# Kernel optimization log

Measured on AMD Instinct MI355X. Metric: run time of the kernel, lower is better.

Reference implementation:

```python
import jax, jax.numpy as jnp
import numpy as np

B, T, S, D, V, NX = 4, 256, 400, 512, 50000, 50
VEXT = V + NX  # extended vocab


def setup_inputs() -> dict:
    key = jax.random.key(0)
    ks = jax.random.split(key, 10)
    s = 0.02
    return {
        "x": jax.random.normal(ks[0], (B, T, D), dtype=jnp.float32),
        "enc_outputs": jax.random.normal(ks[1], (B, S, D), dtype=jnp.float32),
        "src_mask": jax.random.randint(ks[2], (B, 1, S), 0, 2, dtype=jnp.int32),
        "enc_batch_extend_vocab": jax.random.randint(ks[3], (B, S), 0, VEXT, dtype=jnp.int64),
        "extra_zeros": jnp.zeros((B, T, NX), dtype=jnp.float32),
        "fc_w": jax.random.normal(ks[4], (V, D), dtype=jnp.float32) * s,
        "fc_b": jnp.zeros((V,), dtype=jnp.float32),
        "pgen_w": jax.random.normal(ks[5], (1, D), dtype=jnp.float32) * s,
        "pgen_b": jnp.zeros((1,), dtype=jnp.float32),
        "wq": jax.random.normal(ks[6], (D, D), dtype=jnp.float32) * s,
        "bq": jnp.zeros((D,), dtype=jnp.float32),
        "wk": jax.random.normal(ks[7], (D, D), dtype=jnp.float32) * s,
        "bk": jnp.zeros((D,), dtype=jnp.float32),
    }


def reference(x, enc_outputs, src_mask, enc_batch_extend_vocab, extra_zeros,
              fc_w, fc_b, pgen_w, pgen_b, wq, bq, wk, bk):
    # vocab distribution: [B,T,V]
    p_vocab = jax.nn.softmax(x @ fc_w.T + fc_b, axis=-1)
    # single-head cross attention probs (h=1 -> d_k = D)
    q = x @ wq.T + bq                 # [B,T,D]
    k = enc_outputs @ wk.T + bk       # [B,S,D]
    scores = jnp.einsum('btd,bsd->bts', q, k) / jnp.sqrt(jnp.float32(D))
    scores = jnp.where(src_mask == 0, jnp.float32(-1e9), scores)  # mask [B,1,S]
    attn_probs = jax.nn.softmax(scores, axis=-1)  # [B,T,S]
    # generation gate
    p_gen = jax.nn.sigmoid(x @ pgen_w.T + pgen_b)  # [B,T,1]
    attn_dist = (1.0 - p_gen) * attn_probs         # copy distribution over source
    p_ext = jnp.concatenate([p_gen * p_vocab, extra_zeros], axis=-1)  # [B,T,VEXT]
    # scatter-add copy probs into extended vocab slots
    b_idx = jnp.arange(B)[:, None, None]
    t_idx = jnp.arange(T)[None, :, None]
    v_idx = enc_batch_extend_vocab[:, None, :]
    bb, tt, vv = jnp.broadcast_arrays(b_idx, t_idx, v_idx)  # each [B,T,S]
    p_ext = p_ext.at[bb, tt, vv].add(attn_dist)
    return jnp.log(jnp.maximum(p_ext, jnp.float32(1e-9)))
```

## Files before the change

### kernel.cpp

```cpp
#include <hip/hip_runtime.h>
#include <hip/hip_bf16.h>
#include <math.h>

constexpr int cB = 4, cT = 256, cS = 400, cD = 512, cV = 50000, cNX = 50;
constexpr int cVEXT = cV + cNX;
constexpr int cPAN  = (cV + 127) / 128;
constexpr int cMQ   = cB * cT;

typedef __attribute__((ext_vector_type(8))) short short8v;
typedef __attribute__((ext_vector_type(4))) float floatx4;

__device__ inline ushort f2bf(float f) {
    union { float f; unsigned u; } v; v.f = f;
    unsigned r = (v.u + 0x7FFFu + ((v.u >> 16) & 1u)) >> 16;
    return (ushort)r;
}

__global__ __launch_bounds__(256) void cast_kernel(
    const float* __restrict__ src, ushort* __restrict__ dst, int n4)
{
    const int stride = gridDim.x * 256;
    for (int i = blockIdx.x * 256 + threadIdx.x; i < n4; i += stride) {
        float4 v = *(const float4*)(src + (size_t)i * 4);
        ushort4 o;
        o.x = f2bf(v.x); o.y = f2bf(v.y); o.z = f2bf(v.z); o.w = f2bf(v.w);
        *(ushort4*)(dst + (size_t)i * 4) = o;
    }
}

template<bool STATS>
__global__ __launch_bounds__(256) void gemm2(
    const ushort* __restrict__ A, const ushort* __restrict__ Wb,
    const float* __restrict__ bias, float* __restrict__ Cf,
    float* __restrict__ pm, float* __restrict__ ps,
    int M, int N, int K, int ldc)
{
    __shared__ ushort As[2][128 * 32];
    __shared__ ushort Bs[2][128 * 32];
    __shared__ float sm_m[2][128];
    __shared__ float sm_s[2][128];

    const int tid  = threadIdx.x;
    const int lane = tid & 63;
    const int wv   = tid >> 6;
    const int wm   = wv >> 1;
    const int wn   = wv & 1;

    int bm, bn, pan = 0;
    if constexpr (STATS) {
        const int wg  = blockIdx.y * gridDim.x + blockIdx.x;
        const int nwg = gridDim.x * gridDim.y;
        const int j   = (wg & 7) * (nwg >> 3) + (wg >> 3);
        pan = j >> 3;
        bm  = (j & 7) * 128;
        bn  = pan * 128;
    } else {
        bm = blockIdx.x * 128;
        bn = blockIdx.y * 128;
    }

    const int srow = lane >> 2;
    const int sk   = (lane & 3) * 8;

    const int nt = K >> 5;

    floatx4 acc[4][4] = {};

    auto stage = [&](int bidx, int t) {
        const int k0 = t * 32;
        #pragma unroll
        for (int c = 0; c < 2; ++c) {
            const int lr = wv * 32 + c * 16;
            int ga = bm + lr + srow; if (ga >= M) ga = M - 1;
            __builtin_amdgcn_global_load_lds(
                (const __attribute__((address_space(1))) void*)(A + (size_t)ga * K + k0 + sk),
                (__attribute__((address_space(3))) void*)&As[bidx][lr * 32], 16, 0, 0);
        }
        #pragma unroll
        for (int c = 0; c < 2; ++c) {
            const int lr = wv * 32 + c * 16;
            int gb = bn + lr + srow; if (gb >= N) gb = N - 1;
            __builtin_amdgcn_global_load_lds(
                (const __attribute__((address_space(1))) void*)(Wb + (size_t)gb * K + k0 + sk),
                (__attribute__((address_space(3))) void*)&Bs[bidx][lr * 32], 16, 0, 0);
        }
    };

    stage(0, 0);
    __syncthreads();

    const int fr = lane & 15;
    const int g  = lane >> 4;
    int buf = 0;

    for (int t = 0; t < nt; ++t) {
        if (t + 1 < nt) stage(buf ^ 1, t + 1);
        short8v a[4], b[4];
        #pragma unroll
        for (int mi = 0; mi < 4; ++mi)
            a[mi] = *(const short8v*)&As[buf][(wm * 64 + mi * 16 + fr) * 32 + g * 8];
        #pragma unroll
        for (int ni = 0; ni < 4; ++ni)
            b[ni] = *(const short8v*)&Bs[buf][(wn * 64 + ni * 16 + fr) * 32 + g * 8];
        #pragma unroll
        for (int mi = 0; mi < 4; ++mi)
            #pragma unroll
            for (int ni = 0; ni < 4; ++ni)
                acc[mi][ni] = __builtin_amdgcn_mfma_f32_16x16x32_bf16(
                    a[mi], b[ni], acc[mi][ni], 0, 0, 0);
        __syncthreads();
        buf ^= 1;
    }

    float bv[4]; bool val[4];
    #pragma unroll
    for (int ni = 0; ni < 4; ++ni) {
        const int colg = bn + wn * 64 + ni * 16 + fr;
        val[ni] = (colg < N);
        bv[ni] = val[ni] ? bias[colg] : 0.f;
    }
    #pragma unroll
    for (int mi = 0; mi < 4; ++mi)
        #pragma unroll
        for (int ni = 0; ni < 4; ++ni)
            #pragma unroll
            for (int r = 0; r < 4; ++r)
                acc[mi][ni][r] += bv[ni];

    if constexpr (STATS) {
        #pragma unroll
        for (int mi = 0; mi < 4; ++mi) {
            #pragma unroll
            for (int r = 0; r < 4; ++r) {
                float mx = -1e30f;
                #pragma unroll
                for (int ni = 0; ni < 4; ++ni)
                    if (val[ni]) mx = fmaxf(mx, acc[mi][ni][r]);
                #pragma unroll
                for (int sw = 1; sw < 16; sw <<= 1)
                    mx = fmaxf(mx, __shfl_xor(mx, sw));
                float sm = 0.f;
                #pragma unroll
                for (int ni = 0; ni < 4; ++ni)
                    if (val[ni]) sm += __expf(acc[mi][ni][r] - mx);
                #pragma unroll
                for (int sw = 1; sw < 16; sw <<= 1)
                    sm += __shfl_xor(sm, sw);
                if (fr == 0) {
                    const int rl = wm * 64 + mi * 16 + g * 4 + r;
                    sm_m[wn][rl] = mx;
                    sm_s[wn][rl] = sm;
                }
            }
        }
        __syncthreads();
        if (tid < 128) {
            const float m0 = sm_m[0][tid], m1 = sm_m[1][tid];
            const float s0 = sm_s[0][tid], s1 = sm_s[1][tid];
            const float mm = fmaxf(m0, m1);
            const float ss = s0 * __expf(m0 - mm) + s1 * __expf(m1 - mm);
            const int grow = bm + tid;
            if (grow < M) {
                pm[(size_t)pan * M + grow] = mm;
                ps[(size_t)pan * M + grow] = ss;
            }
        }
    }

    #pragma unroll
    for (int mi = 0; mi < 4; ++mi) {
        #pragma unroll
        for (int ni = 0; ni < 4; ++ni) {
            if (!val[ni]) continue;
            const int colg = bn + wn * 64 + ni * 16 + fr;
            #pragma unroll
            for (int r = 0; r < 4; ++r) {
                const int row = bm + wm * 64 + mi * 16 + g * 4 + r;
                if (row < M) Cf[(size_t)row * ldc + colg] = acc[mi][ni][r];
            }
        }
    }
}

__global__ __launch_bounds__(256) void combine_kernel(
    const float* __restrict__ pm, const float* __restrict__ ps,
    const float* __restrict__ pgen, float* __restrict__ rowadd)
{
    const int lane = threadIdx.x & 63;
    const int wv   = threadIdx.x >> 6;
    const int row  = blockIdx.x * 64 + lane;

    float m = -1e30f, s = 0.f;
    #pragma unroll 2
    for (int i = wv; i < cPAN; i += 4) {
        const float mi = pm[(size_t)i * cMQ + row];
        const float si = ps[(size_t)i * cMQ + row];
        const float nm = fmaxf(m, mi);
        s = s * __expf(m - nm) + si * __expf(mi - nm);
        m = nm;
    }
    __shared__ float rm[4][64], rs[4][64];
    rm[wv][lane] = m; rs[wv][lane] = s;
    __syncthreads();
    if (wv == 0) {
        m = rm[0][lane]; s = rs[0][lane];
        #pragma unroll
        for (int i = 1; i < 4; ++i) {
            const float m2 = rm[i][lane], s2 = rs[i][lane];
            const float nm = fmaxf(m, m2);
            s = s * __expf(m - nm) + s2 * __expf(m2 - nm);
            m = nm;
        }
        rowadd[row] = __logf(pgen[row]) - m - __logf(s);
    }
}

__global__ __launch_bounds__(512) void transform_row(
    float* __restrict__ out, const float* __restrict__ rowadd,
    const int* __restrict__ ebev, const float* __restrict__ attn)
{
    const int row = blockIdx.x;
    const int b   = row / cT;
    const int tid = threadIdx.x;
    constexpr float LOGMIN = -20.72326583694641f;

    __shared__ int   pos[cS];
    __shared__ float add[cS];
    for (int s = tid; s < cS; s += 512) {
        pos[s] = ebev[b * cS + s];
        add[s] = attn[(size_t)row * cS + s];
    }

    const float a = rowadd[row];
    float2* rp = (float2*)(out + (size_t)row * cVEXT);
    constexpr int NF2 = cVEXT / 2;
    constexpr int NV2 = cV / 2;
    for (int i = tid; i < NF2; i += 512) {
        float2 o;
        if (i < NV2) {
            float2 v = rp[i];
            o.x = fmaxf(v.x + a, LOGMIN);
            o.y = fmaxf(v.y + a, LOGMIN);
        } else {
            o.x = LOGMIN; o.y = LOGMIN;
        }
        rp[i] = o;
    }
    __syncthreads();

    float* rowf = out + (size_t)row * cVEXT;
    for (int s = tid; s < cS; s += 512) {
        const int p = pos[s];
        bool leader = true;
        for (int s2 = 0; s2 < s; ++s2)
            if (pos[s2] == p) { leader = false; break; }
        if (!leader) continue;
        float sum = add[s];
        for (int s2 = s + 1; s2 < cS; ++s2)
            if (pos[s2] == p) sum += add[s2];
        const float base = __expf(rowf[p]);
        rowf[p] = __logf(fmaxf(base + sum, 1e-9f));
    }
}

__global__ __launch_bounds__(64) void pgen_kernel(
    const float* __restrict__ x, const float* __restrict__ w,
    const float* __restrict__ b, float* __restrict__ pgen)
{
    const int row = blockIdx.x;
    const int lane = threadIdx.x;
    const float* xr = x + (size_t)row * cD;
    float s = 0.f;
    for (int i = lane; i < cD; i += 64) s += xr[i] * w[i];
    #pragma unroll
    for (int off = 32; off; off >>= 1) s += __shfl_down(s, off);
    if (lane == 0) pgen[row] = 1.f / (1.f + __expf(-(s + b[0])));
}

__global__ __launch_bounds__(256) void attn_kernel(
    const float* __restrict__ q, const float* __restrict__ k,
    const int* __restrict__ src_mask, const float* __restrict__ pgen,
    float* __restrict__ attn)
{
    constexpr float scale = 0.04419417382415922f;
    const int row = blockIdx.x;
    const int b = row / cT;
    const int tid = threadIdx.x;

    __shared__ __align__(16) float qs[cD];
    __shared__ float sc[cS];
    __shared__ float red[4];

    for (int i = tid; i < cD; i += 256) qs[i] = q[(size_t)row * cD + i];
    __syncthreads();

    for (int s = tid; s < cS; s += 256) {
        const float* kr = k + ((size_t)b * cS + s) * cD;
        float dot = 0.f;
        #pragma unroll 4
        for (int i = 0; i < cD; i += 4) {
            float4 kv = *(const float4*)(kr + i);
            float4 qv = *(const float4*)(qs + i);
            dot += qv.x * kv.x + qv.y * kv.y + qv.z * kv.z + qv.w * kv.w;
        }
        float v = dot * scale;
        if (src_mask[b * cS + s] == 0) v = -1e9f;
        sc[s] = v;
    }
    __syncthreads();

    float m = -3.4e38f;
    for (int s = tid; s < cS; s += 256) m = fmaxf(m, sc[s]);
    #pragma unroll
    for (int off = 32; off; off >>= 1) m = fmaxf(m, __shfl_down(m, off));
    if ((tid & 63) == 0) red[tid >> 6] = m;
    __syncthreads();
    m = fmaxf(fmaxf(red[0], red[1]), fmaxf(red[2], red[3]));
    __syncthreads();

    float sum = 0.f;
    for (int s = tid; s < cS; s += 256) {
        float e = __expf(sc[s] - m);
        sc[s] = e;
        sum += e;
    }
    #pragma unroll
    for (int off = 32; off; off >>= 1) sum += __shfl_down(sum, off);
    if ((tid & 63) == 0) red[tid >> 6] = sum;
    __syncthreads();
    sum = red[0] + red[1] + red[2] + red[3];

    const float w = (1.f - pgen[row]) / sum;
    for (int s = tid; s < cS; s += 256)
        attn[(size_t)row * cS + s] = sc[s] * w;
}

extern "C" void kernel_launch(void* const* d_in, const int* in_sizes, int n_in,
                              void* d_out, int out_size, void* d_ws, size_t ws_size,
                              hipStream_t stream)
{
    const float* x      = (const float*)d_in[0];
    const float* enc    = (const float*)d_in[1];
    const int*   mask   = (const int*)d_in[2];
    const int*   ebev   = (const int*)d_in[3];
    const float* fc_w   = (const float*)d_in[5];
    const float* fc_b   = (const float*)d_in[6];
    const float* pgen_w = (const float*)d_in[7];
    const float* pgen_b = (const float*)d_in[8];
    const float* wq     = (const float*)d_in[9];
    const float* bq     = (const float*)d_in[10];
    const float* wk     = (const float*)d_in[11];
    const float* bk     = (const float*)d_in[12];
    float* out = (float*)d_out;

    float* ws     = (float*)d_ws;
    float* q      = ws;
    float* kbuf   = q + (size_t)cB * cT * cD;
    float* pgen   = kbuf + (size_t)cB * cS * cD;
    float* attn   = pgen + cB * cT;
    float* pm     = attn + (size_t)cB * cT * cS;
    float* ps     = pm + (size_t)cPAN * cMQ;
    float* rowadd = ps + (size_t)cPAN * cMQ;
    ushort* xb    = (ushort*)(rowadd + cMQ);
    ushort* encb  = xb + (size_t)cB * cT * cD;
    ushort* wqb   = encb + (size_t)cB * cS * cD;
    ushort* wkb   = wqb + (size_t)cD * cD;
    ushort* wb    = wkb + (size_t)cD * cD;

    const dim3 blk(256);
    const int MQ = cMQ;
    const int MK = cB * cS;

    cast_kernel<<<dim3(512), blk, 0, stream>>>(x, xb, (cB * cT * cD) / 4);
    cast_kernel<<<dim3(512), blk, 0, stream>>>(enc, encb, (cB * cS * cD) / 4);
    cast_kernel<<<dim3(256), blk, 0, stream>>>(wq, wqb, (cD * cD) / 4);
    cast_kernel<<<dim3(256), blk, 0, stream>>>(wk, wkb, (cD * cD) / 4);
    cast_kernel<<<dim3(2048), blk, 0, stream>>>(fc_w, wb, (cV * cD) / 4);

    gemm2<false><<<dim3(MQ / 128, cD / 128), blk, 0, stream>>>(
        xb, wqb, bq, q, nullptr, nullptr, MQ, cD, cD, cD);
    gemm2<false><<<dim3((MK + 127) / 128, cD / 128), blk, 0, stream>>>(
        encb, wkb, bk, kbuf, nullptr, nullptr, MK, cD, cD, cD);
    pgen_kernel<<<dim3(MQ), dim3(64), 0, stream>>>(x, pgen_w, pgen_b, pgen);

    attn_kernel<<<dim3(MQ), blk, 0, stream>>>(q, kbuf, mask, pgen, attn);

    gemm2<true><<<dim3(8, cPAN), blk, 0, stream>>>(
        xb, wb, fc_b, out, pm, ps, MQ, cV, cD, cVEXT);

    combine_kernel<<<dim3(MQ / 64), blk, 0, stream>>>(pm, ps, pgen, rowadd);

    transform_row<<<dim3(MQ), dim3(512), 0, stream>>>(out, rowadd, ebev, attn);
}
```

Baseline: 449.9 us.

## Store vocab logits as bf16 in upper half of output row and expand in place

The big vocab GEMM now writes its logits as bf16 into the upper half of each output row's byte range, halving that intermediate write. The transform kernel reads the bf16 values, applies the row offset and clamp, and writes fp32 results into the lower half of the same row. A block-wide barrier between each read and its write guards against overlapping positions in the same row. The GEMM shared-memory staging is also changed to a chunked layout, so each lane loads its MFMA fragment contiguously. Risks are bf16 rounding of the logits before the log output, and correctness that depends on the in-place aliasing order.

Result: no change. 443.5 us (-1.4%).

```diff
diff --git a/kernel.cpp b/kernel.cpp
--- a/kernel.cpp
+++ b/kernel.cpp
@@ -5,6 +5,8 @@
 constexpr int cB = 4, cT = 256, cS = 400, cD = 512, cV = 50000, cNX = 50;
 constexpr int cVEXT = cV + cNX;
 constexpr int cPAN  = (cV + 127) / 128;
+constexpr int cCBLD = cVEXT * 2;
+constexpr int cTOP  = 50100;
 constexpr int cMQ   = cB * cT;
 
 typedef __attribute__((ext_vector_type(8))) short short8v;
@@ -14,6 +16,10 @@
     union { float f; unsigned u; } v; v.f = f;
     unsigned r = (v.u + 0x7FFFu + ((v.u >> 16) & 1u)) >> 16;
     return (ushort)r;
+}
+__device__ inline float bf2f(ushort u) {
+    union { unsigned u; float f; } v; v.u = ((unsigned)u) << 16;
+    return v.f;
 }
 
 __global__ __launch_bounds__(256) void cast_kernel(
@@ -31,7 +37,8 @@
 template<bool STATS>
 __global__ __launch_bounds__(256) void gemm2(
     const ushort* __restrict__ A, const ushort* __restrict__ Wb,
-    const float* __restrict__ bias, float* __restrict__ Cf,
+    const float* __restrict__ bias,
+    float* __restrict__ Cf, ushort* __restrict__ Cb,
     float* __restrict__ pm, float* __restrict__ ps,
     int M, int N, int K, int ldc)
 {
@@ -59,9 +66,8 @@
         bn = blockIdx.y * 128;
     }
 
-    const int srow = lane >> 2;
-    const int sk   = (lane & 3) * 8;
-
+    const int rA = lane & 15;
+    const int kA = (lane >> 4) * 8;
     const int nt = K >> 5;
 
     floatx4 acc[4][4] = {};
@@ -70,19 +76,15 @@
         const int k0 = t * 32;
         #pragma unroll
         for (int c = 0; c < 2; ++c) {
-            const int lr = wv * 32 + c * 16;
-            int ga = bm + lr + srow; if (ga >= M) ga = M - 1;
+            const int chunk = wv * 2 + c;
+            int ga = bm + chunk * 16 + rA; if (ga >= M) ga = M - 1;
             __builtin_amdgcn_global_load_lds(
-                (const __attribute__((address_space(1))) void*)(A + (size_t)ga * K + k0 + sk),
-                (__attribute__((address_space(3))) void*)&As[bidx][lr * 32], 16, 0, 0);
-        }
-        #pragma unroll
-        for (int c = 0; c < 2; ++c) {
-            const int lr = wv * 32 + c * 16;
-            int gb = bn + lr + srow; if (gb >= N) gb = N - 1;
+                (const __attribute__((address_space(1))) void*)(A + (size_t)ga * K + k0 + kA),
+                (__attribute__((address_space(3))) void*)&As[bidx][chunk * 512], 16, 0, 0);
+            int gb = bn + chunk * 16 + rA; if (gb >= N) gb = N - 1;
             __builtin_amdgcn_global_load_lds(
-                (const __attribute__((address_space(1))) void*)(Wb + (size_t)gb * K + k0 + sk),
-                (__attribute__((address_space(3))) void*)&Bs[bidx][lr * 32], 16, 0, 0);
+                (const __attribute__((address_space(1))) void*)(Wb + (size_t)gb * K + k0 + kA),
+                (__attribute__((address_space(3))) void*)&Bs[bidx][chunk * 512], 16, 0, 0);
         }
     };
 
@@ -98,10 +100,10 @@
         short8v a[4], b[4];
         #pragma unroll
         for (int mi = 0; mi < 4; ++mi)
-            a[mi] = *(const short8v*)&As[buf][(wm * 64 + mi * 16 + fr) * 32 + g * 8];
+            a[mi] = *(const short8v*)&As[buf][(wm * 4 + mi) * 512 + lane * 8];
         #pragma unroll
         for (int ni = 0; ni < 4; ++ni)
-            b[ni] = *(const short8v*)&Bs[buf][(wn * 64 + ni * 16 + fr) * 32 + g * 8];
+            b[ni] = *(const short8v*)&Bs[buf][(wn * 4 + ni) * 512 + lane * 8];
         #pragma unroll
         for (int mi = 0; mi < 4; ++mi)
             #pragma unroll
@@ -165,18 +167,31 @@
                 ps[(size_t)pan * M + grow] = ss;
             }
         }
-    }
-
-    #pragma unroll
-    for (int mi = 0; mi < 4; ++mi) {
-        #pragma unroll
-        for (int ni = 0; ni < 4; ++ni) {
-            if (!val[ni]) continue;
-            const int colg = bn + wn * 64 + ni * 16 + fr;
+        #pragma unroll
+        for (int mi = 0; mi < 4; ++mi) {
             #pragma unroll
-            for (int r = 0; r < 4; ++r) {
-                const int row = bm + wm * 64 + mi * 16 + g * 4 + r;
-                if (row < M) Cf[(size_t)row * ldc + colg] = acc[mi][ni][r];
+            for (int ni = 0; ni < 4; ++ni) {
+                if (!val[ni]) continue;
+                const int colg = bn + wn * 64 + ni * 16 + fr;
+                #pragma unroll
+                for (int r = 0; r < 4; ++r) {
+                    const int row = bm + wm * 64 + mi * 16 + g * 4 + r;
+                    Cb[(size_t)row * cCBLD + cTOP + colg] = f2bf(acc[mi][ni][r]);
+                }
+            }
+        }
+    } else {
+        #pragma unroll
+        for (int mi = 0; mi < 4; ++mi) {
+            #pragma unroll
+            for (int ni = 0; ni < 4; ++ni) {
+                if (!val[ni]) continue;
+                const int colg = bn + wn * 64 + ni * 16 + fr;
+                #pragma unroll
+                for (int r = 0; r < 4; ++r) {
+                    const int row = bm + wm * 64 + mi * 16 + g * 4 + r;
+                    if (row < M) Cf[(size_t)row * ldc + colg] = acc[mi][ni][r];
+                }
             }
         }
     }
@@ -215,7 +230,7 @@
     }
 }
 
-__global__ __launch_bounds__(512) void transform_row(
+__global__ __launch_bounds__(512) void transform_reg(
     float* __restrict__ out, const float* __restrict__ rowadd,
     const int* __restrict__ ebev, const float* __restrict__ attn)
 {
@@ -232,23 +247,42 @@
     }
 
     const float a = rowadd[row];
-    float2* rp = (float2*)(out + (size_t)row * cVEXT);
-    constexpr int NF2 = cVEXT / 2;
-    constexpr int NV2 = cV / 2;
-    for (int i = tid; i < NF2; i += 512) {
-        float2 o;
-        if (i < NV2) {
-            float2 v = rp[i];
-            o.x = fmaxf(v.x + a, LOGMIN);
-            o.y = fmaxf(v.y + a, LOGMIN);
-        } else {
-            o.x = LOGMIN; o.y = LOGMIN;
-        }
-        rp[i] = o;
-    }
-    __syncthreads();
-
+    const ushort* rowu = (const ushort*)out + (size_t)row * cCBLD + cTOP;
     float* rowf = out + (size_t)row * cVEXT;
+
+    #pragma unroll 1
+    for (int t = 0; t < 13; ++t) {
+        const int cidx = t * 512 + tid;
+        const bool v = cidx < cV / 8;
+        ushort4 lo = {}, hi = {};
+        if (v) {
+            lo = *(const ushort4*)(rowu + (size_t)cidx * 8);
+            hi = *(const ushort4*)(rowu + (size_t)cidx * 8 + 4);
+        }
+        __syncthreads();
+        if (v) {
+            const int j = cidx * 8;
+            float2 o;
+            o.x = fmaxf(bf2f(lo.x) + a, LOGMIN);
+            o.y = fmaxf(bf2f(lo.y) + a, LOGMIN);
+            *(float2*)(rowf + j) = o;
+            o.x = fmaxf(bf2f(lo.z) + a, LOGMIN);
+            o.y = fmaxf(bf2f(lo.w) + a, LOGMIN);
+            *(float2*)(rowf + j + 2) = o;
+            o.x = fmaxf(bf2f(hi.x) + a, LOGMIN);
+            o.y = fmaxf(bf2f(hi.y) + a, LOGMIN);
+            *(float2*)(rowf + j + 4) = o;
+            o.x = fmaxf(bf2f(hi.z) + a, LOGMIN);
+            o.y = fmaxf(bf2f(hi.w) + a, LOGMIN);
+            *(float2*)(rowf + j + 6) = o;
+        }
+    }
+    if (tid < (cVEXT - cV) / 2) {
+        float2 z; z.x = LOGMIN; z.y = LOGMIN;
+        *(float2*)(rowf + cV + 2 * tid) = z;
+    }
+    __syncthreads();
+
     for (int s = tid; s < cS; s += 512) {
         const int p = pos[s];
         bool leader = true;
@@ -378,17 +412,17 @@
     cast_kernel<<<dim3(2048), blk, 0, stream>>>(fc_w, wb, (cV * cD) / 4);
 
     gemm2<false><<<dim3(MQ / 128, cD / 128), blk, 0, stream>>>(
-        xb, wqb, bq, q, nullptr, nullptr, MQ, cD, cD, cD);
+        xb, wqb, bq, q, nullptr, nullptr, nullptr, MQ, cD, cD, cD);
     gemm2<false><<<dim3((MK + 127) / 128, cD / 128), blk, 0, stream>>>(
-        encb, wkb, bk, kbuf, nullptr, nullptr, MK, cD, cD, cD);
+        encb, wkb, bk, kbuf, nullptr, nullptr, nullptr, MK, cD, cD, cD);
     pgen_kernel<<<dim3(MQ), dim3(64), 0, stream>>>(x, pgen_w, pgen_b, pgen);
 
     attn_kernel<<<dim3(MQ), blk, 0, stream>>>(q, kbuf, mask, pgen, attn);
 
     gemm2<true><<<dim3(8, cPAN), blk, 0, stream>>>(
-        xb, wb, fc_b, out, pm, ps, MQ, cV, cD, cVEXT);
+        xb, wb, fc_b, nullptr, (ushort*)out, pm, ps, MQ, cV, cD, 0);
 
     combine_kernel<<<dim3(MQ / 64), blk, 0, stream>>>(pm, ps, pgen, rowadd);
 
-    transform_row<<<dim3(MQ), dim3(512), 0, stream>>>(out, rowadd, ebev, attn);
-}
+    transform_reg<<<dim3(MQ), dim3(512), 0, stream>>>(out, rowadd, ebev, attn);
+}
```
